# Optimization experiments

Hardware: AMD Instinct MI355X
Metric: run time of the kernel (lower is better)

Reference implementation:

```python
import jax, jax.numpy as jnp
import numpy as np

DROPOUT_P = 0.1
DROPOUT_KEY = 42  # fixed key so the reference is deterministic


def setup_inputs() -> dict:
    key = jax.random.key(0)
    kx, kw = jax.random.split(key)
    B, N, D = 8, 2048, 1024
    x = jax.random.normal(kx, (B, N, D), dtype=jnp.float32)
    # xavier_uniform_ on [D, D]: U(-a, a), a = sqrt(6 / (D + D))
    a = np.sqrt(6.0 / (D + D)).astype(np.float32)
    weight = jax.random.uniform(kw, (D, D), dtype=jnp.float32, minval=-a, maxval=a)
    return {"x": x, "weight": weight}


def reference(x, weight):
    # bilinear scores: (x @ W) @ x^T  -> [B, N, N]
    scores = jnp.einsum("bnd,de,bme->bnm", x, weight, x)
    attn = jax.nn.softmax(scores, axis=-1)
    # dropout (train-mode, inverted scaling), deterministic key
    keep = jax.random.bernoulli(jax.random.key(DROPOUT_KEY), 1.0 - DROPOUT_P, attn.shape)
    attn = jnp.where(keep, attn / (1.0 - DROPOUT_P), 0.0)
    return jnp.einsum("bnm,bmd->bnd", attn, x)
```

## Files before the change

kernel.cpp:

```cpp
#include <hip/hip_runtime.h>
#include <hip/hip_fp16.h>
#include <stdint.h>

typedef __attribute__((ext_vector_type(8))) _Float16 f16x8;
typedef __attribute__((ext_vector_type(4))) float f32x4;
typedef __attribute__((ext_vector_type(8))) short s16x8;

#define MFMA_F16(a, b, c) __builtin_amdgcn_mfma_f32_16x16x32_f16((a), (b), (c), 0, 0, 0)
#define MFMA_BF16(a, b, c) __builtin_amdgcn_mfma_f32_16x16x32_bf16((a), (b), (c), 0, 0, 0)

__device__ __forceinline__ uint32_t pack_hi2(float f0, float f1, float& r0, float& r1) {
  uint32_t b0 = __float_as_uint(f0), b1 = __float_as_uint(f1);
  r0 = f0 - __uint_as_float(b0 & 0xFFFF0000u);
  r1 = f1 - __uint_as_float(b1 & 0xFFFF0000u);
  return (b1 & 0xFFFF0000u) | (b0 >> 16);
}
__device__ __forceinline__ uint32_t pack_lo2(float r0, float r1) {
  return (__float_as_uint(r1) & 0xFFFF0000u) | (__float_as_uint(r0) >> 16);
}
__device__ __forceinline__ uint32_t f16rn(float f) {
  return (uint32_t)__half_as_ushort(__float2half_rn(f));
}
__device__ __forceinline__ float f16tof(uint32_t h) {
  return __half2float(__ushort_as_half((unsigned short)h));
}

__device__ __forceinline__ uint2 threefry2x32_42(uint32_t x0, uint32_t x1) {
  const uint32_t ks0 = 0u, ks1 = 42u, ks2 = 0x1BD11BDAu ^ 42u;
  x0 += ks0; x1 += ks1;
#define TF_R(rot) { x0 += x1; x1 = ((x1 << rot) | (x1 >> (32 - rot))); x1 ^= x0; }
  TF_R(13) TF_R(15) TF_R(26) TF_R(6)   x0 += ks1; x1 += ks2 + 1u;
  TF_R(17) TF_R(29) TF_R(16) TF_R(24)  x0 += ks2; x1 += ks0 + 2u;
  TF_R(13) TF_R(15) TF_R(26) TF_R(6)   x0 += ks0; x1 += ks1 + 3u;
  TF_R(17) TF_R(29) TF_R(16) TF_R(24)  x0 += ks1; x1 += ks2 + 4u;
  TF_R(13) TF_R(15) TF_R(26) TF_R(6)   x0 += ks2; x1 += ks0 + 5u;
#undef TF_R
  return make_uint2(x0, x1);
}
__device__ __forceinline__ bool keep_bit(uint32_t j) {
  uint2 tf = threefry2x32_42(0u, j);
  uint32_t bits = tf.x ^ tf.y;
  return (__uint_as_float(0x3F800000u | (bits >> 9)) - 1.0f) < 0.9f;
}

__global__ __launch_bounds__(256, 3) void bilin_gemm1(
    const float* __restrict__ X, const float* __restrict__ W,
    uint32_t* __restrict__ Ypk) {
  __shared__ uint16_t sAh[128][40];
  __shared__ uint16_t sAl[128][40];
  __shared__ uint16_t sBh[128][40];
  __shared__ uint16_t sBl[128][40];

  const int t = threadIdx.x;
  const int lane = t & 63;
  const int wv = t >> 6;
  const int wm = wv >> 1, wn = wv & 1;
  const int lc = lane & 15, lg = lane >> 4;
  const int M0 = blockIdx.y * 128;
  const int N0 = blockIdx.x * 128;

  const f32x4 fzero = {0.f, 0.f, 0.f, 0.f};
  f32x4 acc[4][4];
#pragma unroll
  for (int i = 0; i < 4; ++i)
#pragma unroll
    for (int j = 0; j < 4; ++j) acc[i][j] = fzero;

  const int ar = t >> 1;
  const int ak = (t & 1) * 16;
  const int bc = t & 127;
  const int bq = t >> 7;

  const float* aptr = X + (size_t)(M0 + ar) * 1024 + ak;
  const float* bptr = W + (size_t)bq * 16 * 1024 + N0 + bc;

  for (int k0 = 0; k0 < 1024; k0 += 32) {
    {
      const float4* s = (const float4*)(aptr + k0);
#pragma unroll
      for (int q = 0; q < 2; ++q) {
        float4 v0 = s[q * 2 + 0];
        float4 v1 = s[q * 2 + 1];
        float r0, r1, r2, r3, r4, r5, r6, r7;
        uint32_t h0 = pack_hi2(v0.x, v0.y, r0, r1);
        uint32_t h1 = pack_hi2(v0.z, v0.w, r2, r3);
        uint32_t h2 = pack_hi2(v1.x, v1.y, r4, r5);
        uint32_t h3 = pack_hi2(v1.z, v1.w, r6, r7);
        uint32_t l0 = pack_lo2(r0, r1), l1 = pack_lo2(r2, r3);
        uint32_t l2 = pack_lo2(r4, r5), l3 = pack_lo2(r6, r7);
        *(uint4*)&sAh[ar][ak + q * 8] = make_uint4(h0, h1, h2, h3);
        *(uint4*)&sAl[ar][ak + q * 8] = make_uint4(l0, l1, l2, l3);
      }
    }
    {
      float v[16];
#pragma unroll
      for (int i = 0; i < 16; ++i) v[i] = bptr[(size_t)(k0 + i) * 1024];
      float r[16];
      uint32_t h[8], lo[8];
#pragma unroll
      for (int i = 0; i < 8; ++i) h[i] = pack_hi2(v[2 * i], v[2 * i + 1], r[2 * i], r[2 * i + 1]);
#pragma unroll
      for (int i = 0; i < 8; ++i) lo[i] = pack_lo2(r[2 * i], r[2 * i + 1]);
      *(uint4*)&sBh[bc][bq * 16 + 0] = make_uint4(h[0], h[1], h[2], h[3]);
      *(uint4*)&sBh[bc][bq * 16 + 8] = make_uint4(h[4], h[5], h[6], h[7]);
      *(uint4*)&sBl[bc][bq * 16 + 0] = make_uint4(lo[0], lo[1], lo[2], lo[3]);
      *(uint4*)&sBl[bc][bq * 16 + 8] = make_uint4(lo[4], lo[5], lo[6], lo[7]);
    }
    __syncthreads();
    s16x8 ah[4], al[4];
#pragma unroll
    for (int mi = 0; mi < 4; ++mi) {
      ah[mi] = *(const s16x8*)&sAh[wm * 64 + mi * 16 + lc][lg * 8];
      al[mi] = *(const s16x8*)&sAl[wm * 64 + mi * 16 + lc][lg * 8];
    }
#pragma unroll
    for (int ni = 0; ni < 4; ++ni) {
      s16x8 bh = *(const s16x8*)&sBh[wn * 64 + ni * 16 + lc][lg * 8];
      s16x8 bl = *(const s16x8*)&sBl[wn * 64 + ni * 16 + lc][lg * 8];
#pragma unroll
      for (int mi = 0; mi < 4; ++mi) {
        acc[mi][ni] = MFMA_BF16(ah[mi], bh, acc[mi][ni]);
        acc[mi][ni] = MFMA_BF16(ah[mi], bl, acc[mi][ni]);
        acc[mi][ni] = MFMA_BF16(al[mi], bh, acc[mi][ni]);
      }
    }
    __syncthreads();
  }
#pragma unroll
  for (int mi = 0; mi < 4; ++mi)
#pragma unroll
    for (int ni = 0; ni < 4; ++ni)
#pragma unroll
      for (int r = 0; r < 4; ++r) {
        float y = acc[mi][ni][r];
        uint32_t hb = f16rn(y);
        uint32_t lb = f16rn(y - f16tof(hb));
        int row = M0 + wm * 64 + mi * 16 + lg * 4 + r;
        int col = N0 + wn * 64 + ni * 16 + lc;
        Ypk[(size_t)row * 1024 + col] = (hb << 16) | lb;
      }
}

__global__ __launch_bounds__(256) void pre_prep(const float* __restrict__ X,
    uint16_t* __restrict__ XhT) {
  __shared__ uint16_t tile[64][72];
  const int t = threadIdx.x;
  const int b = blockIdx.z;
  const int d0 = blockIdx.x * 64;
  const int k0 = blockIdx.y * 64;
  const int rr = t >> 2;
  const int cq = (t & 3) * 16;
  const float* src = X + (size_t)(b * 2048 + k0 + rr) * 1024 + d0 + cq;
#pragma unroll
  for (int q = 0; q < 4; ++q) {
    float4 v = ((const float4*)src)[q];
    tile[cq + q * 4 + 0][rr] = (uint16_t)f16rn(v.x);
    tile[cq + q * 4 + 1][rr] = (uint16_t)f16rn(v.y);
    tile[cq + q * 4 + 2][rr] = (uint16_t)f16rn(v.z);
    tile[cq + q * 4 + 3][rr] = (uint16_t)f16rn(v.w);
  }
  __syncthreads();
  uint16_t* dst = XhT + (size_t)(b * 1024 + d0 + rr) * 2048 + k0 + cq;
  *(uint4*)dst = *(const uint4*)&tile[rr][cq];
  *(uint4*)(dst + 8) = *(const uint4*)&tile[rr][cq + 8];
}

__global__ __launch_bounds__(256, 3) void bilin_score(
    const float* __restrict__ X, const uint32_t* __restrict__ Ypk,
    uint16_t* __restrict__ Sp, float* __restrict__ Mt, float* __restrict__ Psum) {
  __shared__ uint16_t sAh[128][40];
  __shared__ uint16_t sAl[128][40];
  __shared__ uint16_t sBh[128][40];
  __shared__ uint16_t sBl[128][40];
  __shared__ float pm[2][128];
  __shared__ float psr[2][128];
  __shared__ float cm[128];

  const int t = threadIdx.x;
  const int lane = t & 63;
  const int wv = t >> 6;
  const int wm = wv >> 1, wn = wv & 1;
  const int lc = lane & 15, lg = lane >> 4;

  const int bid = blockIdx.x;
  const int b = bid & 7;
  const int tl = bid >> 3;
  const int M0 = (tl & 15) * 128;
  const int ktile = tl >> 4;
  const int N0 = ktile * 128;

  const uint32_t* Yb = Ypk + (size_t)b * 2048 * 1024;
  const float* Xb = X + (size_t)b * 2048 * 1024;

  const f32x4 fzero = {0.f, 0.f, 0.f, 0.f};
  f32x4 acc[4][4];
#pragma unroll
  for (int i = 0; i < 4; ++i)
#pragma unroll
    for (int j = 0; j < 4; ++j) acc[i][j] = fzero;

  const int ar = t >> 1;
  const int ak = (t & 1) * 16;

  for (int k0 = 0; k0 < 1024; k0 += 32) {
    {
      const uint4* as = (const uint4*)&Yb[(size_t)(M0 + ar) * 1024 + k0 + ak];
      uint32_t hp[8], lp[8];
#pragma unroll
      for (int q = 0; q < 4; ++q) {
        uint4 u = as[q];
        hp[q * 2 + 0] = (u.x >> 16) | (u.y & 0xFFFF0000u);
        hp[q * 2 + 1] = (u.z >> 16) | (u.w & 0xFFFF0000u);
        lp[q * 2 + 0] = (u.x & 0xFFFFu) | (u.y << 16);
        lp[q * 2 + 1] = (u.z & 0xFFFFu) | (u.w << 16);
      }
      *(uint4*)&sAh[ar][ak + 0] = make_uint4(hp[0], hp[1], hp[2], hp[3]);
      *(uint4*)&sAh[ar][ak + 8] = make_uint4(hp[4], hp[5], hp[6], hp[7]);
      *(uint4*)&sAl[ar][ak + 0] = make_uint4(lp[0], lp[1], lp[2], lp[3]);
      *(uint4*)&sAl[ar][ak + 8] = make_uint4(lp[4], lp[5], lp[6], lp[7]);
    }
    {
      const float4* bs = (const float4*)&Xb[(size_t)(N0 + ar) * 1024 + k0 + ak];
      uint32_t hp[8], lp[8];
#pragma unroll
      for (int q = 0; q < 4; ++q) {
        float4 v = bs[q];
        uint32_t h0 = f16rn(v.x), h1 = f16rn(v.y), h2 = f16rn(v.z), h3 = f16rn(v.w);
        uint32_t l0 = f16rn(v.x - f16tof(h0));
        uint32_t l1 = f16rn(v.y - f16tof(h1));
        uint32_t l2 = f16rn(v.z - f16tof(h2));
        uint32_t l3 = f16rn(v.w - f16tof(h3));
        hp[q * 2 + 0] = h0 | (h1 << 16);
        hp[q * 2 + 1] = h2 | (h3 << 16);
        lp[q * 2 + 0] = l0 | (l1 << 16);
        lp[q * 2 + 1] = l2 | (l3 << 16);
      }
      *(uint4*)&sBh[ar][ak + 0] = make_uint4(hp[0], hp[1], hp[2], hp[3]);
      *(uint4*)&sBh[ar][ak + 8] = make_uint4(hp[4], hp[5], hp[6], hp[7]);
      *(uint4*)&sBl[ar][ak + 0] = make_uint4(lp[0], lp[1], lp[2], lp[3]);
      *(uint4*)&sBl[ar][ak + 8] = make_uint4(lp[4], lp[5], lp[6], lp[7]);
    }
    __syncthreads();
    f16x8 ah[4], al[4];
#pragma unroll
    for (int mi = 0; mi < 4; ++mi) {
      ah[mi] = *(const f16x8*)&sAh[wm * 64 + mi * 16 + lc][lg * 8];
      al[mi] = *(const f16x8*)&sAl[wm * 64 + mi * 16 + lc][lg * 8];
    }
#pragma unroll
    for (int ni = 0; ni < 4; ++ni) {
      f16x8 bh = *(const f16x8*)&sBh[wn * 64 + ni * 16 + lc][lg * 8];
      f16x8 bl = *(const f16x8*)&sBl[wn * 64 + ni * 16 + lc][lg * 8];
#pragma unroll
      for (int mi = 0; mi < 4; ++mi) {
        acc[mi][ni] = MFMA_F16(ah[mi], bh, acc[mi][ni]);
        acc[mi][ni] = MFMA_F16(ah[mi], bl, acc[mi][ni]);
        acc[mi][ni] = MFMA_F16(al[mi], bh, acc[mi][ni]);
      }
    }
    __syncthreads();
  }

#pragma unroll
  for (int mi = 0; mi < 4; ++mi)
#pragma unroll
    for (int r = 0; r < 4; ++r) {
      float m = fmaxf(fmaxf(acc[mi][0][r], acc[mi][1][r]),
                      fmaxf(acc[mi][2][r], acc[mi][3][r]));
      m = fmaxf(m, __shfl_xor(m, 1, 64));
      m = fmaxf(m, __shfl_xor(m, 2, 64));
      m = fmaxf(m, __shfl_xor(m, 4, 64));
      m = fmaxf(m, __shfl_xor(m, 8, 64));
      if (lc == 0) pm[wn][wm * 64 + mi * 16 + lg * 4 + r] = m;
    }
  __syncthreads();
  if (t < 128) {
    float m = fmaxf(pm[0][t], pm[1][t]);
    cm[t] = m;
    Mt[((size_t)b * 16 + ktile) * 2048 + M0 + t] = m;
  }
  __syncthreads();

  uint16_t* Sb = Sp + (size_t)b * 2048 * 2048;
#pragma unroll
  for (int mi = 0; mi < 4; ++mi)
#pragma unroll
    for (int r = 0; r < 4; ++r) {
      const int rl = wm * 64 + mi * 16 + lg * 4 + r;
      const float m = cm[rl];
      const uint32_t jrow = (uint32_t)b * 4194304u + (uint32_t)(M0 + rl) * 2048u +
                            (uint32_t)(N0 + wn * 64) + (uint32_t)lc;
      float s = 0.0f;
#pragma unroll
      for (int ni = 0; ni < 4; ++ni) {
        float sv = acc[mi][ni][r] - m;
        s += __expf(sv);
        bool kp = keep_bit(jrow + ni * 16u);
        Sb[(size_t)(M0 + rl) * 2048 + N0 + wn * 64 + ni * 16 + lc] =
            kp ? (uint16_t)f16rn(sv) : (uint16_t)0xFC00u;
      }
      s += __shfl_xor(s, 1, 64);
      s += __shfl_xor(s, 2, 64);
      s += __shfl_xor(s, 4, 64);
      s += __shfl_xor(s, 8, 64);
      if (lc == 0) psr[wn][rl] = s;
    }
  __syncthreads();
  if (t < 128)
    Psum[((size_t)b * 16 + ktile) * 2048 + M0 + t] = psr[0][t] + psr[1][t];
}

__global__ __launch_bounds__(1024, 4) void bilin_pv(
    float* __restrict__ YO, const uint16_t* __restrict__ Sp,
    const float* __restrict__ Mt, const float* __restrict__ Psum,
    const uint16_t* __restrict__ XhT) {
  __shared__ __align__(16) uint16_t Pl[2][64][136];
  __shared__ float mts[64][17];
  __shared__ float mrowL[64], invL[64];

  const int t = threadIdx.x;
  const int lane = t & 63;
  const int wv = t >> 6;
  const int lc = lane & 15, lg = lane >> 4;

  const int b = blockIdx.x & 7;
  const int q0 = (blockIdx.x >> 3) * 64;

  const uint16_t* Sb = Sp + (size_t)b * 2048 * 2048;
  const uint16_t* Vb = XhT + (size_t)b * 1024 * 2048;

  const int row = t >> 4;
  const int sub = t & 15;

  {
    float mtv = Mt[((size_t)b * 16 + sub) * 2048 + q0 + row];
    float ps = Psum[((size_t)b * 16 + sub) * 2048 + q0 + row];
    mts[row][sub] = mtv;
    float m = mtv;
    m = fmaxf(m, __shfl_xor(m, 1, 64));
    m = fmaxf(m, __shfl_xor(m, 2, 64));
    m = fmaxf(m, __shfl_xor(m, 4, 64));
    m = fmaxf(m, __shfl_xor(m, 8, 64));
    float sc = ps * __expf(mtv - m);
    sc += __shfl_xor(sc, 1, 64);
    sc += __shfl_xor(sc, 2, 64);
    sc += __shfl_xor(sc, 4, 64);
    sc += __shfl_xor(sc, 8, 64);
    if (sub == 0) { mrowL[row] = m; invL[row] = 1.0f / (sc * 0.9f); }
  }
  __syncthreads();

  const f32x4 fzero = {0.f, 0.f, 0.f, 0.f};
  f32x4 acc[4][4];
#pragma unroll
  for (int i = 0; i < 4; ++i)
#pragma unroll
    for (int j = 0; j < 4; ++j) acc[i][j] = fzero;

  const int d0 = wv * 64;
  const float mrL = mrowL[row];

  auto stage = [&](uint4 su, int kt, int buf) {
    const float mdel = mts[row][kt] - mrL;
    float p0 = __expf(f16tof(su.x & 0xFFFFu) + mdel);
    float p1 = __expf(f16tof(su.x >> 16) + mdel);
    float p2 = __expf(f16tof(su.y & 0xFFFFu) + mdel);
    float p3 = __expf(f16tof(su.y >> 16) + mdel);
    float p4 = __expf(f16tof(su.z & 0xFFFFu) + mdel);
    float p5 = __expf(f16tof(su.z >> 16) + mdel);
    float p6 = __expf(f16tof(su.w & 0xFFFFu) + mdel);
    float p7 = __expf(f16tof(su.w >> 16) + mdel);
    uint32_t w0 = f16rn(p0) | (f16rn(p1) << 16);
    uint32_t w1 = f16rn(p2) | (f16rn(p3) << 16);
    uint32_t w2 = f16rn(p4) | (f16rn(p5) << 16);
    uint32_t w3 = f16rn(p6) | (f16rn(p7) << 16);
    *(uint4*)&Pl[buf][row][sub * 8] = make_uint4(w0, w1, w2, w3);
  };

  uint4 su = *(const uint4*)&Sb[(size_t)(q0 + row) * 2048 + 0 * 128 + sub * 8];
  stage(su, 0, 0);
  __syncthreads();

  for (int kt = 0; kt < 16; ++kt) {
    const int cb = kt & 1;
    uint4 sun;
    if (kt < 15)
      sun = *(const uint4*)&Sb[(size_t)(q0 + row) * 2048 + (kt + 1) * 128 + sub * 8];
#pragma unroll
    for (int kst = 0; kst < 4; ++kst) {
      f16x8 a0 = *(const f16x8*)&Pl[cb][0 * 16 + lc][kst * 32 + lg * 8];
      f16x8 a1 = *(const f16x8*)&Pl[cb][1 * 16 + lc][kst * 32 + lg * 8];
      f16x8 a2 = *(const f16x8*)&Pl[cb][2 * 16 + lc][kst * 32 + lg * 8];
      f16x8 a3 = *(const f16x8*)&Pl[cb][3 * 16 + lc][kst * 32 + lg * 8];
#pragma unroll
      for (int nc = 0; nc < 4; ++nc) {
        f16x8 v = *(const f16x8*)&Vb[(size_t)(d0 + nc * 16 + lc) * 2048 +
                                     kt * 128 + kst * 32 + lg * 8];
        acc[0][nc] = MFMA_F16(a0, v, acc[0][nc]);
        acc[1][nc] = MFMA_F16(a1, v, acc[1][nc]);
        acc[2][nc] = MFMA_F16(a2, v, acc[2][nc]);
        acc[3][nc] = MFMA_F16(a3, v, acc[3][nc]);
      }
    }
    if (kt < 15) stage(sun, kt + 1, cb ^ 1);
    __syncthreads();
  }

  float* outb = YO + (size_t)b * 2048 * 1024;
#pragma unroll
  for (int fr = 0; fr < 4; ++fr)
#pragma unroll
    for (int r = 0; r < 4; ++r) {
      const int rl = fr * 16 + lg * 4 + r;
      const float inv = invL[rl];
#pragma unroll
      for (int nc = 0; nc < 4; ++nc)
        outb[(size_t)(q0 + rl) * 1024 + d0 + nc * 16 + lc] = acc[fr][nc][r] * inv;
    }
}

__global__ __launch_bounds__(512, 4) void bilin_flash2f(
    const float* __restrict__ X, float* __restrict__ YO) {
  __shared__ __align__(16) uint16_t kbuf[2][2][128][40];
  __shared__ __align__(16) uint16_t qbuf[2][2][32][40];
  __shared__ __align__(16) uint16_t Pl[32][136];
  __shared__ float red[8][16];
  __shared__ float mrow[32], lrow[32], frow[32];
  uint16_t* vbase = &kbuf[0][0][0][0];

  const int t = threadIdx.x;
  const int lane = t & 63;
  const int wv = t >> 6;
  const int wr = wv >> 2, wc = wv & 3;
  const int lc = lane & 15, lg = lane >> 4;
  const int b = blockIdx.x & 7;
  const int q0 = (blockIdx.x >> 3) * 32;

  const float* Xb = X + (size_t)b * 2048 * 1024;
  const uint32_t* Ypk = (const uint32_t*)YO;

  if (t < 32) { mrow[t] = -1e30f; lrow[t] = 0.0f; }

  const f32x4 fzero = {0.f, 0.f, 0.f, 0.f};
  f32x4 acc_pv[16];
#pragma unroll
  for (int c = 0; c < 16; ++c) acc_pv[c] = fzero;

  const int myrow = wr * 16 + lg * 4;
  const int qsr = t >> 3;
  const int qsc = (t & 7) * 4;
  const int ksk = t >> 2;
  const int ksd = (t & 3) * 8;
  const int vkp = t & 63;
  const int vdg = t >> 6;

  for (int kb = 0; kb < 16; ++kb) {
    const int kbase = kb * 128;
    __syncthreads();

    f32x4 acc_s0 = fzero, acc_s1 = fzero;
    uint4 qld;
    float4 kf0, kf1;

    auto load_q = [&](int dd) {
      if (t < 256) qld = *(const uint4*)&Ypk[(size_t)(b * 2048 + q0 + qsr) * 1024 + dd + qsc];
    };
    auto write_q = [&](int nb) {
      if (t < 256) {
        uint32_t hh0 = (qld.x >> 16) | (qld.y & 0xFFFF0000u);
        uint32_t hh1 = (qld.z >> 16) | (qld.w & 0xFFFF0000u);
        uint32_t ll0 = (qld.x & 0xFFFFu) | (qld.y << 16);
        uint32_t ll1 = (qld.z & 0xFFFFu) | (qld.w << 16);
        *(uint2*)&qbuf[nb][0][qsr][qsc] = make_uint2(hh0, hh1);
        *(uint2*)&qbuf[nb][1][qsr][qsc] = make_uint2(ll0, ll1);
      }
    };
    auto load_k = [&](int dd) {
      const float* s = &Xb[(size_t)(kbase + ksk) * 1024 + dd + ksd];
      kf0 = ((const float4*)s)[0];
      kf1 = ((const float4*)s)[1];
    };
    auto write_k = [&](int nb) {
      float e[8] = {kf0.x, kf0.y, kf0.z, kf0.w, kf1.x, kf1.y, kf1.z, kf1.w};
      uint32_t h[8], l[8];
#pragma unroll
      for (int j = 0; j < 8; ++j) {
        h[j] = f16rn(e[j]);
        l[j] = f16rn(e[j] - f16tof(h[j]));
      }
      *(uint4*)&kbuf[nb][0][ksk][ksd] =
          make_uint4(h[0] | (h[1] << 16), h[2] | (h[3] << 16), h[4] | (h[5] << 16), h[6] | (h[7] << 16));
      *(uint4*)&kbuf[nb][1][ksk][ksd] =
          make_uint4(l[0] | (l[1] << 16), l[2] | (l[3] << 16), l[4] | (l[5] << 16), l[6] | (l[7] << 16));
    };

    load_q(0); load_k(0);
    write_q(0); write_k(0);
    __syncthreads();
#pragma unroll 2
    for (int dc = 0; dc < 32; ++dc) {
      const int cb = dc & 1;
      if (dc < 31) { load_q((dc + 1) * 32); load_k((dc + 1) * 32); }
      f16x8 ah = *(const f16x8*)&qbuf[cb][0][wr * 16 + lc][lg * 8];
      f16x8 al = *(const f16x8*)&qbuf[cb][1][wr * 16 + lc][lg * 8];
      {
        f16x8 bh = *(const f16x8*)&kbuf[cb][0][wc * 32 + lc][lg * 8];
        f16x8 bl = *(const f16x8*)&kbuf[cb][1][wc * 32 + lc][lg * 8];
        acc_s0 = MFMA_F16(ah, bh, acc_s0);
        acc_s0 = MFMA_F16(ah, bl, acc_s0);
        acc_s0 = MFMA_F16(al, bh, acc_s0);
      }
      {
        f16x8 bh = *(const f16x8*)&kbuf[cb][0][wc * 32 + 16 + lc][lg * 8];
        f16x8 bl = *(const f16x8*)&kbuf[cb][1][wc * 32 + 16 + lc][lg * 8];
        acc_s1 = MFMA_F16(ah, bh, acc_s1);
        acc_s1 = MFMA_F16(ah, bl, acc_s1);
        acc_s1 = MFMA_F16(al, bh, acc_s1);
      }
      if (dc < 31) { write_q(cb ^ 1); write_k(cb ^ 1); __syncthreads(); }
    }

#pragma unroll
    for (int r = 0; r < 4; ++r) {
      float m = fmaxf(acc_s0[r], acc_s1[r]);
      m = fmaxf(m, __shfl_xor(m, 1, 64));
      m = fmaxf(m, __shfl_xor(m, 2, 64));
      m = fmaxf(m, __shfl_xor(m, 4, 64));
      m = fmaxf(m, __shfl_xor(m, 8, 64));
      if (lc == 0) red[wv][lg * 4 + r] = m;
    }
    __syncthreads();
    if (t < 32) {
      int wrr = t >> 4, rr = t & 15;
      float mk = fmaxf(fmaxf(red[wrr * 4 + 0][rr], red[wrr * 4 + 1][rr]),
                       fmaxf(red[wrr * 4 + 2][rr], red[wrr * 4 + 3][rr]));
      float mo = mrow[t], mn = fmaxf(mo, mk);
      mrow[t] = mn;
      frow[t] = __expf(mo - mn);
    }
    __syncthreads();
#pragma unroll
    for (int r = 0; r < 4; ++r) {
      const int row = myrow + r;
      const float mn = mrow[row];
      float p0 = __expf(acc_s0[r] - mn);
      float p1 = __expf(acc_s1[r] - mn);
      float s = p0 + p1;
      s += __shfl_xor(s, 1, 64);
      s += __shfl_xor(s, 2, 64);
      s += __shfl_xor(s, 4, 64);
      s += __shfl_xor(s, 8, 64);
      if (lc == 0) red[wv][lg * 4 + r] = s;
      uint32_t jr = (uint32_t)b * 4194304u + (uint32_t)(q0 + row) * 2048u +
                    (uint32_t)(kbase + wc * 32 + lc);
      bool k0 = keep_bit(jr);
      bool k1 = keep_bit(jr + 16u);
      Pl[row][wc * 32 + lc] = k0 ? (uint16_t)f16rn(p0) : (uint16_t)0;
      Pl[row][wc * 32 + 16 + lc] = k1 ? (uint16_t)f16rn(p1) : (uint16_t)0;
    }
    __syncthreads();
    if (t < 32) {
      int wrr = t >> 4, rr = t & 15;
      lrow[t] = lrow[t] * frow[t] + (red[wrr * 4 + 0][rr] + red[wrr * 4 + 1][rr] +
                                     red[wrr * 4 + 2][rr] + red[wrr * 4 + 3][rr]);
    }

    {
      float fr[4];
#pragma unroll
      for (int r = 0; r < 4; ++r) fr[r] = frow[myrow + r];
#pragma unroll
      for (int c = 0; c < 16; ++c)
#pragma unroll
        for (int r = 0; r < 4; ++r) acc_pv[c][r] *= fr[r];
    }
    f16x8 ap0 = *(const f16x8*)&Pl[wr * 16 + lc][0 * 32 + lg * 8];
    f16x8 ap1 = *(const f16x8*)&Pl[wr * 16 + lc][1 * 32 + lg * 8];
    f16x8 ap2 = *(const f16x8*)&Pl[wr * 16 + lc][2 * 32 + lg * 8];
    f16x8 ap3 = *(const f16x8*)&Pl[wr * 16 + lc][3 * 32 + lg * 8];

    float4 vf0, vf1, vf2, vf3;
    auto load_v = [&](int c) {
      const float* s0 = &Xb[(size_t)(kbase + vkp * 2) * 1024 + c * 64 + vdg * 8];
      vf0 = ((const float4*)s0)[0];
      vf1 = ((const float4*)s0)[1];
      vf2 = ((const float4*)(s0 + 1024))[0];
      vf3 = ((const float4*)(s0 + 1024))[1];
    };
    auto write_v = [&](int nb) {
      uint16_t* vt = vbase + nb * (64 * 136);
      float a[8] = {vf0.x, vf0.y, vf0.z, vf0.w, vf1.x, vf1.y, vf1.z, vf1.w};
      float b2[8] = {vf2.x, vf2.y, vf2.z, vf2.w, vf3.x, vf3.y, vf3.z, vf3.w};
#pragma unroll
      for (int j = 0; j < 8; ++j)
        *(uint32_t*)&vt[(vdg * 8 + j) * 136 + vkp * 2] = f16rn(a[j]) | (f16rn(b2[j]) << 16);
    };

    load_v(0); write_v(0);
    __syncthreads();
#pragma unroll
    for (int c = 0; c < 16; ++c) {
      const int cb = c & 1;
      if (c < 15) load_v(c + 1);
      const uint16_t* vt = vbase + cb * (64 * 136);
      f16x8 bf0 = *(const f16x8*)&vt[(wc * 16 + lc) * 136 + 0 * 32 + lg * 8];
      f16x8 bf1 = *(const f16x8*)&vt[(wc * 16 + lc) * 136 + 1 * 32 + lg * 8];
      f16x8 bf2 = *(const f16x8*)&vt[(wc * 16 + lc) * 136 + 2 * 32 + lg * 8];
      f16x8 bf3 = *(const f16x8*)&vt[(wc * 16 + lc) * 136 + 3 * 32 + lg * 8];
      acc_pv[c] = MFMA_F16(ap0, bf0, acc_pv[c]);
      acc_pv[c] = MFMA_F16(ap1, bf1, acc_pv[c]);
      acc_pv[c] = MFMA_F16(ap2, bf2, acc_pv[c]);
      acc_pv[c] = MFMA_F16(ap3, bf3, acc_pv[c]);
      if (c < 15) { write_v(cb ^ 1); __syncthreads(); }
    }
  }

  __syncthreads();
  float inv[4];
#pragma unroll
  for (int r = 0; r < 4; ++r) inv[r] = 1.0f / (lrow[myrow + r] * 0.9f);
  float* outb = YO + (size_t)b * 2048 * 1024;
#pragma unroll
  for (int c = 0; c < 16; ++c)
#pragma unroll
    for (int r = 0; r < 4; ++r)
      outb[(size_t)(q0 + myrow + r) * 1024 + c * 64 + wc * 16 + lc] = acc_pv[c][r] * inv[r];
}

extern "C" void kernel_launch(void* const* d_in, const int* in_sizes, int n_in,
                              void* d_out, int out_size, void* d_ws, size_t ws_size,
                              hipStream_t stream) {
  (void)in_sizes; (void)n_in; (void)out_size;
  const float* X = (const float*)d_in[0];
  const float* W = (const float*)d_in[1];
  const bool usews = ws_size >= 104857600ULL;

  bilin_gemm1<<<dim3(8, 128), 256, 0, stream>>>(X, W, (uint32_t*)d_out);

  if (usews) {
    uint16_t* XhT = (uint16_t*)d_ws;
    uint16_t* Sp = (uint16_t*)((char*)d_ws + 33554432);
    float* Mt = (float*)((char*)d_ws + 33554432 + 67108864);
    float* Psum = (float*)((char*)d_ws + 33554432 + 67108864 + 1048576);
    pre_prep<<<dim3(16, 32, 8), 256, 0, stream>>>(X, XhT);
    bilin_score<<<2048, 256, 0, stream>>>(X, (const uint32_t*)d_out, Sp, Mt, Psum);
    bilin_pv<<<256, 1024, 0, stream>>>((float*)d_out, Sp, Mt, Psum, XhT);
  } else {
    bilin_flash2f<<<512, 512, 0, stream>>>(X, (float*)d_out);
  }
}
```

Measured before the change: 583.0 us.

## Pre-split and transpose W once, drop X low-part MFMA in score kernel

Adds a small kernel that splits W into transposed bf16 hi/lo planes so the first GEMM loads contiguous uint4 rows instead of strided scalar floats and skips per-tile splitting. The score kernel stops computing and storing the fp16 low residual of X, removing one of three MFMAs per tile and one LDS buffer, which lets occupancy go to 4 blocks. This lowers the accuracy of the scores. The workspace is reused: WhT/WlT alias Mt/Psum, which is safe only because gemm1 finishes before score writes Mt.

```diff
diff --git a/kernel.cpp b/kernel.cpp
--- a/kernel.cpp
+++ b/kernel.cpp
@@ -43,9 +43,39 @@
   return (__uint_as_float(0x3F800000u | (bits >> 9)) - 1.0f) < 0.9f;
 }
 
-__global__ __launch_bounds__(256, 3) void bilin_gemm1(
-    const float* __restrict__ X, const float* __restrict__ W,
-    uint32_t* __restrict__ Ypk) {
+__global__ __launch_bounds__(256) void w_splitT(const float* __restrict__ W,
+    uint16_t* __restrict__ WhT, uint16_t* __restrict__ WlT) {
+  __shared__ uint16_t th[64][72];
+  __shared__ uint16_t tl[64][72];
+  const int t = threadIdx.x;
+  const int n0 = blockIdx.x * 64;
+  const int k0 = blockIdx.y * 64;
+  const int rr = t >> 2;
+  const int cq = (t & 3) * 16;
+  const float* src = W + (size_t)(k0 + rr) * 1024 + n0 + cq;
+#pragma unroll
+  for (int q = 0; q < 4; ++q) {
+    float4 v = ((const float4*)src)[q];
+    float e[4] = {v.x, v.y, v.z, v.w};
+#pragma unroll
+    for (int j = 0; j < 4; ++j) {
+      uint32_t b = __float_as_uint(e[j]);
+      float rem = e[j] - __uint_as_float(b & 0xFFFF0000u);
+      th[cq + q * 4 + j][rr] = (uint16_t)(b >> 16);
+      tl[cq + q * 4 + j][rr] = (uint16_t)(__float_as_uint(rem) >> 16);
+    }
+  }
+  __syncthreads();
+  size_t dst = (size_t)(n0 + rr) * 1024 + k0 + cq;
+  *(uint4*)&WhT[dst] = *(const uint4*)&th[rr][cq];
+  *(uint4*)&WhT[dst + 8] = *(const uint4*)&th[rr][cq + 8];
+  *(uint4*)&WlT[dst] = *(const uint4*)&tl[rr][cq];
+  *(uint4*)&WlT[dst + 8] = *(const uint4*)&tl[rr][cq + 8];
+}
+
+__global__ __launch_bounds__(256, 3) void bilin_gemm1w(
+    const float* __restrict__ X, const uint16_t* __restrict__ WhT,
+    const uint16_t* __restrict__ WlT, uint32_t* __restrict__ Ypk) {
   __shared__ uint16_t sAh[128][40];
   __shared__ uint16_t sAl[128][40];
   __shared__ uint16_t sBh[128][40];
@@ -72,7 +102,8 @@
   const int bq = t >> 7;
 
   const float* aptr = X + (size_t)(M0 + ar) * 1024 + ak;
-  const float* bptr = W + (size_t)bq * 16 * 1024 + N0 + bc;
+  const uint16_t* whp = WhT + (size_t)(N0 + bc) * 1024 + bq * 16;
+  const uint16_t* wlp = WlT + (size_t)(N0 + bc) * 1024 + bq * 16;
 
   for (int k0 = 0; k0 < 1024; k0 += 32) {
     {
@@ -93,19 +124,10 @@
       }
     }
     {
-      float v[16];
-#pragma unroll
-      for (int i = 0; i < 16; ++i) v[i] = bptr[(size_t)(k0 + i) * 1024];
-      float r[16];
-      uint32_t h[8], lo[8];
-#pragma unroll
-      for (int i = 0; i < 8; ++i) h[i] = pack_hi2(v[2 * i], v[2 * i + 1], r[2 * i], r[2 * i + 1]);
-#pragma unroll
-      for (int i = 0; i < 8; ++i) lo[i] = pack_lo2(r[2 * i], r[2 * i + 1]);
-      *(uint4*)&sBh[bc][bq * 16 + 0] = make_uint4(h[0], h[1], h[2], h[3]);
-      *(uint4*)&sBh[bc][bq * 16 + 8] = make_uint4(h[4], h[5], h[6], h[7]);
-      *(uint4*)&sBl[bc][bq * 16 + 0] = make_uint4(lo[0], lo[1], lo[2], lo[3]);
-      *(uint4*)&sBl[bc][bq * 16 + 8] = make_uint4(lo[4], lo[5], lo[6], lo[7]);
+      *(uint4*)&sBh[bc][bq * 16 + 0] = ((const uint4*)(whp + k0))[0];
+      *(uint4*)&sBh[bc][bq * 16 + 8] = ((const uint4*)(whp + k0))[1];
+      *(uint4*)&sBl[bc][bq * 16 + 0] = ((const uint4*)(wlp + k0))[0];
+      *(uint4*)&sBl[bc][bq * 16 + 8] = ((const uint4*)(wlp + k0))[1];
     }
     __syncthreads();
     s16x8 ah[4], al[4];
@@ -166,13 +188,12 @@
   *(uint4*)(dst + 8) = *(const uint4*)&tile[rr][cq + 8];
 }
 
-__global__ __launch_bounds__(256, 3) void bilin_score(
+__global__ __launch_bounds__(256, 4) void bilin_score(
     const float* __restrict__ X, const uint32_t* __restrict__ Ypk,
     uint16_t* __restrict__ Sp, float* __restrict__ Mt, float* __restrict__ Psum) {
   __shared__ uint16_t sAh[128][40];
   __shared__ uint16_t sAl[128][40];
   __shared__ uint16_t sBh[128][40];
-  __shared__ uint16_t sBl[128][40];
   __shared__ float pm[2][128];
   __shared__ float psr[2][128];
   __shared__ float cm[128];
@@ -222,24 +243,15 @@
     }
     {
       const float4* bs = (const float4*)&Xb[(size_t)(N0 + ar) * 1024 + k0 + ak];
-      uint32_t hp[8], lp[8];
+      uint32_t hp[8];
 #pragma unroll
       for (int q = 0; q < 4; ++q) {
         float4 v = bs[q];
-        uint32_t h0 = f16rn(v.x), h1 = f16rn(v.y), h2 = f16rn(v.z), h3 = f16rn(v.w);
-        uint32_t l0 = f16rn(v.x - f16tof(h0));
-        uint32_t l1 = f16rn(v.y - f16tof(h1));
-        uint32_t l2 = f16rn(v.z - f16tof(h2));
-        uint32_t l3 = f16rn(v.w - f16tof(h3));
-        hp[q * 2 + 0] = h0 | (h1 << 16);
-        hp[q * 2 + 1] = h2 | (h3 << 16);
-        lp[q * 2 + 0] = l0 | (l1 << 16);
-        lp[q * 2 + 1] = l2 | (l3 << 16);
+        hp[q * 2 + 0] = f16rn(v.x) | (f16rn(v.y) << 16);
+        hp[q * 2 + 1] = f16rn(v.z) | (f16rn(v.w) << 16);
       }
       *(uint4*)&sBh[ar][ak + 0] = make_uint4(hp[0], hp[1], hp[2], hp[3]);
       *(uint4*)&sBh[ar][ak + 8] = make_uint4(hp[4], hp[5], hp[6], hp[7]);
-      *(uint4*)&sBl[ar][ak + 0] = make_uint4(lp[0], lp[1], lp[2], lp[3]);
-      *(uint4*)&sBl[ar][ak + 8] = make_uint4(lp[4], lp[5], lp[6], lp[7]);
     }
     __syncthreads();
     f16x8 ah[4], al[4];
@@ -251,11 +263,9 @@
 #pragma unroll
     for (int ni = 0; ni < 4; ++ni) {
       f16x8 bh = *(const f16x8*)&sBh[wn * 64 + ni * 16 + lc][lg * 8];
-      f16x8 bl = *(const f16x8*)&sBl[wn * 64 + ni * 16 + lc][lg * 8];
 #pragma unroll
       for (int mi = 0; mi < 4; ++mi) {
         acc[mi][ni] = MFMA_F16(ah[mi], bh, acc[mi][ni]);
-        acc[mi][ni] = MFMA_F16(ah[mi], bl, acc[mi][ni]);
         acc[mi][ni] = MFMA_F16(al[mi], bh, acc[mi][ni]);
       }
     }
@@ -418,6 +428,105 @@
       for (int nc = 0; nc < 4; ++nc)
         outb[(size_t)(q0 + rl) * 1024 + d0 + nc * 16 + lc] = acc[fr][nc][r] * inv;
     }
+}
+
+__global__ __launch_bounds__(256, 3) void bilin_gemm1(
+    const float* __restrict__ X, const float* __restrict__ W,
+    uint32_t* __restrict__ Ypk) {
+  __shared__ uint16_t sAh[128][40];
+  __shared__ uint16_t sAl[128][40];
+  __shared__ uint16_t sBh[128][40];
+  __shared__ uint16_t sBl[128][40];
+
+  const int t = threadIdx.x;
+  const int lane = t & 63;
+  const int wv = t >> 6;
+  const int wm = wv >> 1, wn = wv & 1;
+  const int lc = lane & 15, lg = lane >> 4;
+  const int M0 = blockIdx.y * 128;
+  const int N0 = blockIdx.x * 128;
+
+  const f32x4 fzero = {0.f, 0.f, 0.f, 0.f};
+  f32x4 acc[4][4];
+#pragma unroll
+  for (int i = 0; i < 4; ++i)
+#pragma unroll
+    for (int j = 0; j < 4; ++j) acc[i][j] = fzero;
+
+  const int ar = t >> 1;
+  const int ak = (t & 1) * 16;
+  const int bc = t & 127;
+  const int bq = t >> 7;
+
+  const float* aptr = X + (size_t)(M0 + ar) * 1024 + ak;
+  const float* bptr = W + (size_t)bq * 16 * 1024 + N0 + bc;
+
+  for (int k0 = 0; k0 < 1024; k0 += 32) {
+    {
+      const float4* s = (const float4*)(aptr + k0);
+#pragma unroll
+      for (int q = 0; q < 2; ++q) {
+        float4 v0 = s[q * 2 + 0];
+        float4 v1 = s[q * 2 + 1];
+        float r0, r1, r2, r3, r4, r5, r6, r7;
+        uint32_t h0 = pack_hi2(v0.x, v0.y, r0, r1);
+        uint32_t h1 = pack_hi2(v0.z, v0.w, r2, r3);
+        uint32_t h2 = pack_hi2(v1.x, v1.y, r4, r5);
+        uint32_t h3 = pack_hi2(v1.z, v1.w, r6, r7);
+        uint32_t l0 = pack_lo2(r0, r1), l1 = pack_lo2(r2, r3);
+        uint32_t l2 = pack_lo2(r4, r5), l3 = pack_lo2(r6, r7);
+        *(uint4*)&sAh[ar][ak + q * 8] = make_uint4(h0, h1, h2, h3);
+        *(uint4*)&sAl[ar][ak + q * 8] = make_uint4(l0, l1, l2, l3);
+      }
+    }
+    {
+      float v[16];
+#pragma unroll
+      for (int i = 0; i < 16; ++i) v[i] = bptr[(size_t)(k0 + i) * 1024];
+      float r[16];
+      uint32_t h[8], lo[8];
+#pragma unroll
+      for (int i = 0; i < 8; ++i) h[i] = pack_hi2(v[2 * i], v[2 * i + 1], r[2 * i], r[2 * i + 1]);
+#pragma unroll
+      for (int i = 0; i < 8; ++i) lo[i] = pack_lo2(r[2 * i], r[2 * i + 1]);
+      *(uint4*)&sBh[bc][bq * 16 + 0] = make_uint4(h[0], h[1], h[2], h[3]);
+      *(uint4*)&sBh[bc][bq * 16 + 8] = make_uint4(h[4], h[5], h[6], h[7]);
+      *(uint4*)&sBl[bc][bq * 16 + 0] = make_uint4(lo[0], lo[1], lo[2], lo[3]);
+      *(uint4*)&sBl[bc][bq * 16 + 8] = make_uint4(lo[4], lo[5], lo[6], lo[7]);
+    }
+    __syncthreads();
+    s16x8 ah[4], al[4];
+#pragma unroll
+    for (int mi = 0; mi < 4; ++mi) {
+      ah[mi] = *(const s16x8*)&sAh[wm * 64 + mi * 16 + lc][lg * 8];
+      al[mi] = *(const s16x8*)&sAl[wm * 64 + mi * 16 + lc][lg * 8];
+    }
+#pragma unroll
+    for (int ni = 0; ni < 4; ++ni) {
+      s16x8 bh = *(const s16x8*)&sBh[wn * 64 + ni * 16 + lc][lg * 8];
+      s16x8 bl = *(const s16x8*)&sBl[wn * 64 + ni * 16 + lc][lg * 8];
+#pragma unroll
+      for (int mi = 0; mi < 4; ++mi) {
+        acc[mi][ni] = MFMA_BF16(ah[mi], bh, acc[mi][ni]);
+        acc[mi][ni] = MFMA_BF16(ah[mi], bl, acc[mi][ni]);
+        acc[mi][ni] = MFMA_BF16(al[mi], bh, acc[mi][ni]);
+      }
+    }
+    __syncthreads();
+  }
+#pragma unroll
+  for (int mi = 0; mi < 4; ++mi)
+#pragma unroll
+    for (int ni = 0; ni < 4; ++ni)
+#pragma unroll
+      for (int r = 0; r < 4; ++r) {
+        float y = acc[mi][ni][r];
+        uint32_t hb = f16rn(y);
+        uint32_t lb = f16rn(y - f16tof(hb));
+        int row = M0 + wm * 64 + mi * 16 + lg * 4 + r;
+        int col = N0 + wn * 64 + ni * 16 + lc;
+        Ypk[(size_t)row * 1024 + col] = (hb << 16) | lb;
+      }
 }
 
 __global__ __launch_bounds__(512, 4) void bilin_flash2f(
@@ -636,17 +745,20 @@
   const float* W = (const float*)d_in[1];
   const bool usews = ws_size >= 104857600ULL;
 
-  bilin_gemm1<<<dim3(8, 128), 256, 0, stream>>>(X, W, (uint32_t*)d_out);
-
   if (usews) {
     uint16_t* XhT = (uint16_t*)d_ws;
     uint16_t* Sp = (uint16_t*)((char*)d_ws + 33554432);
-    float* Mt = (float*)((char*)d_ws + 33554432 + 67108864);
-    float* Psum = (float*)((char*)d_ws + 33554432 + 67108864 + 1048576);
+    uint16_t* WhT = (uint16_t*)((char*)d_ws + 100663296);
+    uint16_t* WlT = (uint16_t*)((char*)d_ws + 100663296 + 2097152);
+    float* Mt = (float*)((char*)d_ws + 100663296);
+    float* Psum = (float*)((char*)d_ws + 100663296 + 1048576);
+    w_splitT<<<dim3(16, 16), 256, 0, stream>>>(W, WhT, WlT);
+    bilin_gemm1w<<<dim3(8, 128), 256, 0, stream>>>(X, WhT, WlT, (uint32_t*)d_out);
     pre_prep<<<dim3(16, 32, 8), 256, 0, stream>>>(X, XhT);
     bilin_score<<<2048, 256, 0, stream>>>(X, (const uint32_t*)d_out, Sp, Mt, Psum);
     bilin_pv<<<256, 1024, 0, stream>>>((float*)d_out, Sp, Mt, Psum, XhT);
   } else {
+    bilin_gemm1<<<dim3(8, 128), 256, 0, stream>>>(X, W, (uint32_t*)d_out);
     bilin_flash2f<<<512, 512, 0, stream>>>(X, (float*)d_out);
   }
 }
```

After: 573.9 us. About the same (-1.6%).
